# Kernel tuning notes

Hardware: AMD Instinct MI355X
Metric: run time of the kernel (lower is better)

Reference implementation:

```python
import jax, jax.numpy as jnp
import numpy as np

NC = 2            # num_classes
CONF_THR = 0.7
IOU_THR = 0.2

_PI, _PJ = np.triu_indices(9, k=1)   # 36 candidate edge directions for min-area rect


def _decode_level(out, stride):
    # out: [C,h,w]; scale (x,y) channels by stride and add the pixel grid, flatten to [h*w, C]
    C, h, w = out.shape
    gw = (stride * jnp.arange(w, dtype=out.dtype))[None, :]
    gh = (stride * jnp.arange(h, dtype=out.dtype))[:, None]
    out = out.at[NC + 1].set(out[NC + 1] * stride + gw)
    out = out.at[NC + 2].set(out[NC + 2] * stride + gh)
    return out.reshape(C, -1).T


def _min_area_polygons(pts18):
    # pts18: (N,18) interleaved (a,b) coordinate pairs of 9 points.
    # Min-area enclosing rectangle: optimal rect is aligned with some point-pair direction;
    # brute-force all 36 pairs (superset of hull edges) -> exact result, fully vectorized.
    P = pts18.reshape(-1, 9, 2)                       # (N,9,2)
    d = P[:, _PJ] - P[:, _PI]                         # (N,36,2)
    nrm = jnp.sqrt(jnp.sum(d * d, -1) + 1e-12)
    c, s = d[..., 0] / nrm, d[..., 1] / nrm           # (N,36)
    a, b = P[..., 0][:, None, :], P[..., 1][:, None, :]   # (N,1,9)
    u = a * c[..., None] + b * s[..., None]           # rotate by -theta
    v = -a * s[..., None] + b * c[..., None]
    umin, umax = u.min(-1), u.max(-1)
    vmin, vmax = v.min(-1), v.max(-1)
    area = (umax - umin) * (vmax - vmin)              # (N,36)
    k = jnp.argmin(area, 1)[:, None]
    tk = lambda z: jnp.take_along_axis(z, k, 1)[:, 0]
    c, s, umin, umax, vmin, vmax = map(tk, (c, s, umin, umax, vmin, vmax))
    cu = jnp.stack([umin, umax, umax, umin], -1)      # rect corners in rotated frame
    cv = jnp.stack([vmin, vmin, vmax, vmax], -1)
    ca = cu * c[:, None] - cv * s[:, None]            # rotate back
    cb = cu * s[:, None] + cv * c[:, None]
    return jnp.stack([ca, cb], -1).reshape(-1, 8)     # (N,8) interleaved corners


def _points_in_quad(pts, quad):
    # pts (M,2), quad (4,2) convex with consistent winding -> (M,) bool
    e = jnp.roll(quad, -1, 0) - quad
    r = pts[:, None, :] - quad[None]
    cr = e[None, :, 0] * r[..., 1] - e[None, :, 1] * r[..., 0]
    return (cr >= 0).all(-1) | (cr <= 0).all(-1)


def _box_decoder(rect):
    # rect (N,8) -> (N,5) [cx, cy, w, h, angle]; y_first=True convention from the source
    w = jnp.sqrt((rect[:, 0] - rect[:, 2]) ** 2 + (rect[:, 1] - rect[:, 3]) ** 2)
    h = jnp.sqrt((rect[:, 4] - rect[:, 2]) ** 2 + (rect[:, 5] - rect[:, 3]) ** 2)
    cx = rect[:, 1:8:2].sum(1) * 0.25
    cy = rect[:, 0:8:2].sum(1) * 0.25
    ang = jnp.arctan((rect[:, 0] - rect[:, 2]) / (rect[:, 1] - rect[:, 3]))
    return jnp.stack([cx, cy, w, h, ang], -1)


def _rbox_corners(b):
    cx, cy, w, h, a = b[0], b[1], b[2], b[3], b[4]
    cs, sn = jnp.cos(a), jnp.sin(a)
    lx = jnp.array([-0.5, 0.5, 0.5, -0.5]) * w
    ly = jnp.array([-0.5, -0.5, 0.5, 0.5]) * h
    return jnp.stack([cx + lx * cs - ly * sn, cy + lx * sn + ly * cs], -1)  # (4,2)


def _quad_inter_area(A, B):
    # exact intersection area of two convex quads A,B (4,2):
    # candidates = corners of each inside the other + all 16 edge-edge intersections,
    # sorted by angle around their centroid, masked shoelace.
    inA = _points_in_quad(B, A)
    inB = _points_in_quad(A, B)
    rA = jnp.roll(A, -1, 0) - A
    rB = jnp.roll(B, -1, 0) - B
    qp = B[None] - A[:, None]                                  # (4,4,2)
    den = rA[:, None, 0] * rB[None, :, 1] - rA[:, None, 1] * rB[None, :, 0]
    dsafe = jnp.where(jnp.abs(den) < 1e-9, 1e-9, den)
    t = (qp[..., 0] * rB[None, :, 1] - qp[..., 1] * rB[None, :, 0]) / dsafe
    uu = (qp[..., 0] * rA[:, None, 1] - qp[..., 1] * rA[:, None, 0]) / dsafe
    okx = (jnp.abs(den) > 1e-9) & (t >= 0) & (t <= 1) & (uu >= 0) & (uu <= 1)
    X = A[:, None] + t[..., None] * rA[:, None]
    pts = jnp.concatenate([A, B, X.reshape(16, 2)], 0)          # (24,2)
    val = jnp.concatenate([inB, inA, okx.reshape(16)], 0)
    n = val.sum()
    cen = jnp.sum(jnp.where(val[:, None], pts, 0.0), 0) / jnp.maximum(n, 1)
    rel = pts - cen
    ang = jnp.where(val, jnp.arctan2(rel[:, 1], rel[:, 0]), 1e9)
    o = jnp.argsort(ang)
    rp, vs = rel[o], val[o]
    rp = jnp.where(vs[:, None], rp, rp[0])   # invalid slots -> first valid vertex (zero-area edges)
    nx = jnp.roll(rp, -1, 0)
    area = 0.5 * jnp.abs(jnp.sum(rp[:, 0] * nx[:, 1] - rp[:, 1] * nx[:, 0]))
    return jnp.where(n >= 3, area, 0.0)


def _forward(out3, out4, out5, off1_l3, off1_l4, off1_l5, offf_l3, offf_l4, offf_l5):
    outs = jnp.concatenate([_decode_level(out3[0], 4),
                            _decode_level(out4[0], 8),
                            _decode_level(out5[0], 16)], 0)          # (N, NC+3)
    flat = lambda z: z[0].reshape(18, -1).T
    off1 = jnp.concatenate([flat(off1_l3), flat(off1_l4), flat(off1_l5)], 0)
    offf = jnp.concatenate([flat(offf_l3), flat(offf_l4), flat(offf_l5)], 0) + off1
    N = outs.shape[0]
    x, y = outs[:, NC + 1], outs[:, NC + 2]
    offf = offf + jnp.tile(jnp.stack([y, x], -1), (1, 9))            # (y,x) interleaved, 9 points
    xs, ys = offf[:, 1:18:2], offf[:, 0:18:2]
    area = (xs.max(1) - xs.min(1)) * (ys.max(1) - ys.min(1)) / 40.0
    conf = outs[:, 0]
    conf_mask = conf > CONF_THR * jax.nn.sigmoid(area)
    rect = _min_area_polygons(offf)                                  # (N,8)
    boxes5 = _box_decoder(rect)                                      # (N,5)
    corners = jax.vmap(_rbox_corners)(boxes5)                        # (N,4,2)
    areas5 = boxes5[:, 2] * boxes5[:, 3]
    position = outs[:, NC + 1:]                                      # (N,2) = (x,y)
    pts_yx = jnp.stack([position[:, 1], position[:, 0]], -1)         # (y,x), matches rect plane
    quads = rect.reshape(N, 4, 2)
    order = jnp.argsort(jnp.where(conf_mask, conf, -jnp.inf))[::-1]

    def step(carry, i):
        suppressed, keep = carry
        active = jnp.logical_not(suppressed[i])
        keep = keep.at[i].set(active)
        inside = _points_in_quad(pts_yx, quads[i])                   # points_in_polygons
        inter = jax.vmap(lambda C: _quad_inter_area(corners[i], C))(corners)
        iou = inter / (areas5[i] + areas5 - inter + 1e-9)            # box_iou_rotated
        suppressed = suppressed | (active & (inside | (iou >= IOU_THR)))
        return (suppressed, keep), None

    init = (jnp.logical_not(conf_mask), jnp.zeros(N, dtype=bool))
    (_, keep), _ = jax.lax.scan(step, init, order)

    cls = outs[:, 1:NC + 1]
    maxc = cls.max(1)
    masks = jnp.stack([keep & (cls[:, i] == maxc) for i in range(NC)], 0)  # (NC,N)
    cnt = masks.sum(1)
    result = jnp.where(masks[:, :, None], position[None], 0.0)             # (NC,N,2) padded
    rect_out = rect * keep[:, None].astype(rect.dtype)                     # (N,8) padded
    return cnt, result, rect_out


def setup_inputs() -> dict:
    key = jax.random.key(0)
    shapes = [("out3", (1, NC + 3, 32, 32)), ("out4", (1, NC + 3, 16, 16)), ("out5", (1, NC + 3, 8, 8)),
              ("off1_l3", (1, 18, 32, 32)), ("off1_l4", (1, 18, 16, 16)), ("off1_l5", (1, 18, 8, 8)),
              ("offf_l3", (1, 18, 32, 32)), ("offf_l4", (1, 18, 16, 16)), ("offf_l5", (1, 18, 8, 8))]
    ks = jax.random.split(key, len(shapes))
    return {n: jax.random.normal(k, s, dtype=jnp.float32) for (n, s), k in zip(shapes, ks)}


def reference(out3, out4, out5, off1_l3, off1_l4, off1_l5, offf_l3, offf_l4, offf_l5):
    return _forward(out3, out4, out5, off1_l3, off1_l4, off1_l5, offf_l3, offf_l4, offf_l5)
```

## Files before the change

kernel.cpp:

```cpp
#include <hip/hip_runtime.h>
#include <math.h>

#define N_DET 1344
#define MW_MAX 8
#define T2S 9
#define QCAP 2048


__device__ __forceinline__ bool pt_in_quad4(const float* qx, const float* qy,
                                            float px, float py) {
    bool allp = true, alln = true;
#pragma unroll
    for (int k = 0; k < 4; k++) {
        int k1 = (k + 1) & 3;
        float ex = qx[k1] - qx[k], ey = qy[k1] - qy[k];
        float rx = px - qx[k],     ry = py - qy[k];
        float cr = ex * ry - ey * rx;
        allp = allp && (cr >= 0.f);
        alln = alln && (cr <= 0.f);
    }
    return allp || alln;
}

__device__ float quad_inter_area(const float* Ax, const float* Ay,
                                 const float* Bx, const float* By) {
    float px[24], py[24];
    unsigned vmask = 0;
    int n = 0;
#pragma unroll
    for (int k = 0; k < 4; k++) {
        px[k] = Ax[k]; py[k] = Ay[k];
        if (pt_in_quad4(Bx, By, Ax[k], Ay[k])) { vmask |= 1u << k; n++; }
    }
#pragma unroll
    for (int k = 0; k < 4; k++) {
        px[4 + k] = Bx[k]; py[4 + k] = By[k];
        if (pt_in_quad4(Ax, Ay, Bx[k], By[k])) { vmask |= 1u << (4 + k); n++; }
    }
#pragma unroll
    for (int k = 0; k < 4; k++) {
        int k1 = (k + 1) & 3;
        float rax = Ax[k1] - Ax[k], ray = Ay[k1] - Ay[k];
#pragma unroll
        for (int l = 0; l < 4; l++) {
            int l1 = (l + 1) & 3;
            float rbx = Bx[l1] - Bx[l], rby = By[l1] - By[l];
            float qpx = Bx[l] - Ax[k],  qpy = By[l] - Ay[k];
            float den = rax * rby - ray * rbx;
            float ad  = fabsf(den);
            float dsafe = (ad < 1e-9f) ? 1e-9f : den;
            float t = (qpx * rby - qpy * rbx) / dsafe;
            float u = (qpx * ray - qpy * rax) / dsafe;
            bool ok = (ad > 1e-9f) && t >= 0.f && t <= 1.f && u >= 0.f && u <= 1.f;
            int id = 8 + k * 4 + l;
            px[id] = Ax[k] + t * rax;
            py[id] = Ay[k] + t * ray;
            if (ok) { vmask |= 1u << id; n++; }
        }
    }
    float cx = 0.f, cy = 0.f;
#pragma unroll
    for (int m = 0; m < 24; m++)
        if ((vmask >> m) & 1u) { cx += px[m]; cy += py[m]; }
    int mx = (n < 1) ? 1 : n;
    cx = cx / (float)mx;
    cy = cy / (float)mx;

    unsigned long long key[32];
    float sx[32], sy[32];
#pragma unroll
    for (int m = 0; m < 24; m++) {
        float rx = px[m] - cx, ry = py[m] - cy;
        float a = ((vmask >> m) & 1u) ? atan2f(ry, rx) : 1e9f;
        unsigned u = __float_as_uint(a);
        u = (u & 0x80000000u) ? ~u : (u | 0x80000000u);
        key[m] = (((unsigned long long)u) << 6) | (unsigned)m;
        sx[m] = rx; sy[m] = ry;
    }
#pragma unroll
    for (int m = 24; m < 32; m++) { key[m] = ~0ull; sx[m] = 0.f; sy[m] = 0.f; }

#pragma unroll
    for (int k = 2; k <= 32; k <<= 1) {
#pragma unroll
        for (int j = k >> 1; j > 0; j >>= 1) {
#pragma unroll
            for (int t = 0; t < 32; t++) {
                int l = t ^ j;
                if (l > t) {
                    bool up = ((t & k) == 0);
                    bool sw = up ? (key[t] > key[l]) : (key[t] < key[l]);
                    if (sw) {
                        unsigned long long tk = key[t]; key[t] = key[l]; key[l] = tk;
                        float tx = sx[t]; sx[t] = sx[l]; sx[l] = tx;
                        float ty = sy[t]; sy[t] = sy[l]; sy[l] = ty;
                    }
                }
            }
        }
    }

    unsigned ut = __float_as_uint(1e9f) | 0x80000000u;
    unsigned long long kt = ((unsigned long long)ut) << 6;
    float fx = sx[0], fy = sy[0];
    float qx2[24], qy2[24];
#pragma unroll
    for (int m = 0; m < 24; m++) {
        bool v = key[m] < kt;
        qx2[m] = v ? sx[m] : fx;
        qy2[m] = v ? sy[m] : fy;
    }
    float ssum = 0.f;
#pragma unroll
    for (int m = 0; m < 24; m++) {
        int m1 = (m + 1) % 24;
        ssum += qx2[m] * qy2[m1] - qy2[m] * qx2[m1];
    }
    float area = 0.5f * fabsf(ssum);
    return (n >= 3) ? area : 0.f;
}

__device__ bool iou_suppress_c(const float* __restrict__ co_cor,
                               const float* __restrict__ co_a5, int p, int q) {
    float Axr[4], Ayr[4], Bxr[4], Byr[4];
#pragma unroll
    for (int k = 0; k < 4; k++) {
        Axr[k] = co_cor[p * 8 + 2 * k]; Ayr[k] = co_cor[p * 8 + 2 * k + 1];
        Bxr[k] = co_cor[q * 8 + 2 * k]; Byr[k] = co_cor[q * 8 + 2 * k + 1];
    }
    float inter = quad_inter_area(Axr, Ayr, Bxr, Byr);
    float iou = inter / (co_a5[p] + co_a5[q] - inter + 1e-9f);
    return iou >= 0.2f;
}

__device__ __forceinline__ int sum_mcount(const int* __restrict__ mcount_w) {
    int M = 0;
#pragma unroll
    for (int k = 0; k < 21; k++) M += mcount_w[k];
    return M;
}

__global__ void k_decode(const float* __restrict__ out3, const float* __restrict__ out4,
                         const float* __restrict__ out5,
                         const float* __restrict__ o1l3, const float* __restrict__ o1l4,
                         const float* __restrict__ o1l5,
                         const float* __restrict__ ofl3, const float* __restrict__ ofl4,
                         const float* __restrict__ ofl5,
                         float* keyArr, float* cls0, float* cls1, float* xx, float* yy,
                         float* a5, float* ccx, float* ccy, float* rr,
                         float* rect, float* cor, int* mcount_w) {
    int n = blockIdx.x * blockDim.x + threadIdx.x;
    if (n >= N_DET) return;
    const float *out, *o1, *of;
    int w, idx; float stride;
    if (n < 1024)      { out = out3; o1 = o1l3; of = ofl3; w = 32; idx = n;        stride = 4.f; }
    else if (n < 1280) { out = out4; o1 = o1l4; of = ofl4; w = 16; idx = n - 1024; stride = 8.f; }
    else               { out = out5; o1 = o1l5; of = ofl5; w = 8;  idx = n - 1280; stride = 16.f; }
    int hw = w * w;
    int row = idx / w, col = idx % w;
    float cf = out[0 * hw + idx];
    float c0 = out[1 * hw + idx];
    float c1 = out[2 * hw + idx];
    float x  = out[3 * hw + idx] * stride + stride * (float)col;
    float y  = out[4 * hw + idx] * stride + stride * (float)row;

    float Pa[9], Pb[9];
    float minb = INFINITY, maxb = -INFINITY, mina = INFINITY, maxa = -INFINITY;
#pragma unroll
    for (int k = 0; k < 9; k++) {
        float a = of[(2 * k) * hw + idx]     + o1[(2 * k) * hw + idx]     + y;
        float b = of[(2 * k + 1) * hw + idx] + o1[(2 * k + 1) * hw + idx] + x;
        Pa[k] = a; Pb[k] = b;
        mina = fminf(mina, a); maxa = fmaxf(maxa, a);
        minb = fminf(minb, b); maxb = fmaxf(maxb, b);
    }
    float area = (maxb - minb) * (maxa - mina) / 40.0f;
    float sg = 1.0f / (1.0f + expf(-area));
    int m = (cf > 0.7f * sg) ? 1 : 0;

    float best = INFINITY, bc = 0.f, bs = 0.f;
    float bumin = 0.f, bumax = 0.f, bvmin = 0.f, bvmax = 0.f;
#pragma unroll
    for (int i = 0; i < 9; i++) {
#pragma unroll
        for (int j = i + 1; j < 9; j++) {
            float d0 = Pa[j] - Pa[i], d1 = Pb[j] - Pb[i];
            float nr = sqrtf(d0 * d0 + d1 * d1 + 1e-12f);
            float c = d0 / nr, s = d1 / nr;
            float umin = INFINITY, umax = -INFINITY, vmin = INFINITY, vmax = -INFINITY;
#pragma unroll
            for (int k = 0; k < 9; k++) {
                float u =  Pa[k] * c + Pb[k] * s;
                float v = -Pa[k] * s + Pb[k] * c;
                umin = fminf(umin, u); umax = fmaxf(umax, u);
                vmin = fminf(vmin, v); vmax = fmaxf(vmax, v);
            }
            float ar = (umax - umin) * (vmax - vmin);
            if (ar < best) { best = ar; bc = c; bs = s;
                             bumin = umin; bumax = umax; bvmin = vmin; bvmax = vmax; }
        }
    }
    float cu[4] = {bumin, bumax, bumax, bumin};
    float cv[4] = {bvmin, bvmin, bvmax, bvmax};
    float r8[8];
#pragma unroll
    for (int k = 0; k < 4; k++) {
        r8[2 * k]     = cu[k] * bc - cv[k] * bs;
        r8[2 * k + 1] = cu[k] * bs + cv[k] * bc;
    }
    float w5 = sqrtf((r8[0] - r8[2]) * (r8[0] - r8[2]) + (r8[1] - r8[3]) * (r8[1] - r8[3]));
    float h5 = sqrtf((r8[4] - r8[2]) * (r8[4] - r8[2]) + (r8[5] - r8[3]) * (r8[5] - r8[3]));
    float cx = (r8[1] + r8[3] + r8[5] + r8[7]) * 0.25f;
    float cy = (r8[0] + r8[2] + r8[4] + r8[6]) * 0.25f;
    float ang = atanf((r8[0] - r8[2]) / (r8[1] - r8[3]));
    float cs = cosf(ang), sn = sinf(ang);
    const float lxs[4] = {-0.5f, 0.5f, 0.5f, -0.5f};
    const float lys[4] = {-0.5f, -0.5f, 0.5f, 0.5f};
#pragma unroll
    for (int k = 0; k < 4; k++) {
        cor[n * 8 + 2 * k]     = cx + lxs[k] * w5 * cs - lys[k] * h5 * sn;
        cor[n * 8 + 2 * k + 1] = cy + lxs[k] * w5 * sn + lys[k] * h5 * cs;
    }
#pragma unroll
    for (int k = 0; k < 8; k++) rect[n * 8 + k] = r8[k];
    keyArr[n] = m ? cf : -INFINITY;
    cls0[n] = c0; cls1[n] = c1;
    xx[n] = x; yy[n] = y; a5[n] = w5 * h5;
    ccx[n] = cx; ccy[n] = cy;
    rr[n] = 0.5f * sqrtf(w5 * w5 + h5 * h5);
    unsigned long long mb = __ballot(m != 0);
    if ((threadIdx.x & 63) == 0) mcount_w[n >> 6] = (int)__popcll(mb);
}

__global__ __launch_bounds__(256) void k_order(
        const float* __restrict__ keyArr,
        const float* __restrict__ xx, const float* __restrict__ yy,
        const float* __restrict__ a5, const float* __restrict__ ccx,
        const float* __restrict__ ccy, const float* __restrict__ rr,
        const float* __restrict__ rect, const float* __restrict__ cor,
        int* order,
        float* co_ccx, float* co_ccy, float* co_rr, float* co_a5,
        float* co_xx, float* co_yy, float* co_rect, float* co_cor) {
    int lane = threadIdx.x & 63;
    int b = blockIdx.x * 4 + (threadIdx.x >> 6);
    float ki = keyArr[b];
    int rank = 0;
    for (int j = lane; j < N_DET; j += 64) {
        float kj = keyArr[j];
        rank += ((kj > ki) || (kj == ki && j > b)) ? 1 : 0;
    }
    for (int off = 32; off; off >>= 1) rank += __shfl_down(rank, off, 64);
    rank = __shfl(rank, 0, 64);
    if (lane == 0)           order[rank] = b;
    if (lane < 8)            co_cor[rank * 8 + lane]        = cor[b * 8 + lane];
    else if (lane < 16)      co_rect[rank * 8 + (lane - 8)] = rect[b * 8 + (lane - 8)];
    else if (lane == 16)     co_ccx[rank] = ccx[b];
    else if (lane == 17)     co_ccy[rank] = ccy[b];
    else if (lane == 18)     co_rr[rank]  = rr[b];
    else if (lane == 19)     co_a5[rank]  = a5[b];
    else if (lane == 20)     co_xx[rank]  = xx[b];
    else if (lane == 21)     co_yy[rank]  = yy[b];
}

__global__ __launch_bounds__(256) void k_pairs(
        const float* __restrict__ co_rect, const float* __restrict__ co_cor,
        const float* __restrict__ co_a5,
        const float* __restrict__ co_xx, const float* __restrict__ co_yy,
        const float* __restrict__ co_ccx, const float* __restrict__ co_ccy,
        const float* __restrict__ co_rr,
        const int* __restrict__ mcount_w, unsigned long long* __restrict__ S2) {
    __shared__ unsigned int queue[QCAP];
    __shared__ int qn;
    int M = sum_mcount(mcount_w);
    int MW = (M + 63) >> 6;
    bool fast = (MW <= MW_MAX);
    int tid = threadIdx.x;
    int lane = tid & 63;
    if (tid == 0) qn = 0;
    __syncthreads();

    if (M > 0) {
        int gwave = (blockIdx.x * 256 + tid) >> 6;
        int nwave = (gridDim.x * 256) >> 6;
        int total = M * MW;
        for (int t = gwave; t < total; t += nwave) {
            int p = t / MW;
            int w = t - p * MW;
            int q = w * 64 + lane;
            bool valid = q < M;
            int qc = valid ? q : 0;

            float cbi = co_ccx[p], cai = co_ccy[p], ri = co_rr[p];
            float pjy = co_yy[qc], pjx = co_xx[qc];
            float da = pjy - cai, db = pjx - cbi;
            float rin = ri + 0.1f;
            bool inside = false;
            if (da * da + db * db <= rin * rin) {
                float qxr[4], qyr[4];
#pragma unroll
                for (int k = 0; k < 4; k++) { qxr[k] = co_rect[p * 8 + 2 * k]; qyr[k] = co_rect[p * 8 + 2 * k + 1]; }
                inside = pt_in_quad4(qxr, qyr, pjy, pjx);
            }
            bool bit = valid && inside;
            unsigned long long bb = __ballot(bit);

            float ex = cbi - co_ccx[qc], ey = cai - co_ccy[qc];
            float rs = ri + co_rr[qc] + 0.1f;
            bool needy = valid && (q != p) && !bit && (ex * ex + ey * ey <= rs * rs);

            if (fast) {
                if (lane == 0) S2[p * MW + w] = bb;
                unsigned long long pm = __ballot(needy);
                if (pm) {
                    int cw = __popcll(pm);
                    int base = 0;
                    if (lane == 0) base = atomicAdd(&qn, cw);
                    base = __shfl(base, 0, 64);
                    if (needy) {
                        int pos = base + __popcll(pm & ((1ull << lane) - 1ull));
                        if (pos < QCAP) {
                            queue[pos] = ((unsigned)p << 11) | (unsigned)q;
                        } else {
                            __threadfence();
                            if (iou_suppress_c(co_cor, co_a5, p, q))
                                atomicOr(&S2[p * MW + w], 1ull << (q & 63));
                        }
                    }
                }
            } else {
                bool supp = needy && iou_suppress_c(co_cor, co_a5, p, q);
                unsigned long long sb = __ballot(supp);
                if (lane == 0) S2[p * MW + w] = bb | sb;
            }
        }
    }
    __syncthreads();

    if (M > 0 && fast) {
        int cnt = qn; if (cnt > QCAP) cnt = QCAP;
        for (int t = tid; t < cnt; t += 256) {
            unsigned v = queue[t];
            int p = (int)(v >> 11), q = (int)(v & 2047u);
            if (iou_suppress_c(co_cor, co_a5, p, q))
                atomicOr(&S2[p * MW + (q >> 6)], 1ull << (q & 63));
        }
    }
}

__global__ __launch_bounds__(512) void k_scan_out(
    const float* __restrict__ cls0, const float* __restrict__ cls1,
    const float* __restrict__ xx, const float* __restrict__ yy,
    const float* __restrict__ rect,
    const int* __restrict__ order, const int* __restrict__ mcount_w,
    const unsigned long long* __restrict__ S2, float* __restrict__ out) {
    __shared__ unsigned long long T2[512 * T2S];
    __shared__ unsigned long long Kfin[MW_MAX];
    __shared__ unsigned int keep32[(N_DET + 31) / 32];
    __shared__ int cnt_s[2];
    int tid = threadIdx.x;
    int lane = tid & 63, wid = tid >> 6;
    int M = sum_mcount(mcount_w);
    int MW = (M + 63) >> 6;
    for (int t = tid; t < (N_DET + 31) / 32; t += 512) keep32[t] = 0u;
    if (tid < 2) cnt_s[tid] = 0;
    if (tid < MW_MAX) Kfin[tid] = 0ull;
    __syncthreads();

    if (M > 0 && MW <= MW_MAX) {
        for (int blk = wid; blk < MW * MW; blk += 8) {
            int wp = blk / MW, wq = blk - wp * MW;
            int pp = wp * 64 + lane;
            unsigned long long x = (pp < M) ? S2[pp * MW + wq] : 0ull;
#pragma unroll
            for (int b = 0; b < 64; b++) {
                unsigned long long bb = __ballot((x >> b) & 1ull);
                if (lane == b) T2[(wq * 64 + b) * T2S + wp] = bb;
            }
        }
        __syncthreads();

        if (wid == 0) {
            unsigned long long kw[MW_MAX];
            unsigned long long pmask = lane ? ((1ull << lane) - 1ull) : 0ull;
#pragma unroll
            for (int k = 0; k < MW_MAX; k++) {
                if (k < MW) {
                    int q = k * 64 + lane;
                    const unsigned long long* row = &T2[q * T2S];
                    unsigned long long base = 0ull;
#pragma unroll
                    for (int w = 0; w < MW_MAX; w++)
                        if (w < k) base |= row[w] & kw[w];
                    unsigned long long rk = row[k] & pmask;
                    bool qv = q < M;
                    int lo = k * 64;
                    unsigned long long cur =
                        (M - lo >= 64) ? ~0ull : ((1ull << (M - lo)) - 1ull);
                    for (int guard = 0; guard < 66; guard++) {
                        bool nb = qv && ((base | (rk & cur)) == 0ull);
                        unsigned long long nw = __ballot(nb);
                        if (nw == cur) break;
                        cur = nw;
                    }
                    kw[k] = cur;
                }
            }
            if (lane == 0) {
#pragma unroll
                for (int w = 0; w < MW_MAX; w++) Kfin[w] = (w < MW) ? kw[w] : 0ull;
            }
        }
        __syncthreads();
        for (int t = tid; t < M; t += 512) {
            if ((Kfin[t >> 6] >> (t & 63)) & 1ull) {
                int i = order[t];
                atomicOr(&keep32[i >> 5], 1u << (i & 31));
            }
        }
    } else if (M > 0) {
        if (wid == 0) {
            unsigned long long rem = 0ull;
            int lo = lane * 64;
            if (M > lo) rem = (M - lo >= 64) ? ~0ull : ((1ull << (M - lo)) - 1ull);
            for (int guard = 0; guard < N_DET; guard++) {
                unsigned long long vote = __ballot(rem != 0ull);
                if (!vote) break;
                int w = __builtin_ctzll(vote);
                unsigned long long wd = __shfl(rem, w, 64);
                int b = __builtin_ctzll(wd);
                int p = w * 64 + b;
                int i = order[p];
                if (lane == 0) atomicOr(&keep32[i >> 5], 1u << (i & 31));
                unsigned long long rowv = (lane < MW) ? S2[p * MW + lane] : 0ull;
                rem &= ~rowv;
                if (lane == w) rem &= ~(1ull << b);
            }
        }
    }
    __syncthreads();

    int c0 = 0, c1 = 0;
    for (int n = tid; n < N_DET; n += 512) {
        bool kp = (keep32[n >> 5] >> (n & 31)) & 1u;
        float a = cls0[n], b = cls1[n];
        float mxc = fmaxf(a, b);
        bool m0 = kp && (a == mxc);
        bool m1 = kp && (b == mxc);
        float x = xx[n], y = yy[n];
        out[2 + 0 * N_DET * 2 + n * 2 + 0] = m0 ? x : 0.f;
        out[2 + 0 * N_DET * 2 + n * 2 + 1] = m0 ? y : 0.f;
        out[2 + 1 * N_DET * 2 + n * 2 + 0] = m1 ? x : 0.f;
        out[2 + 1 * N_DET * 2 + n * 2 + 1] = m1 ? y : 0.f;
        float kf = kp ? 1.f : 0.f;
#pragma unroll
        for (int k = 0; k < 8; k++)
            out[2 + 2 * N_DET * 2 + n * 8 + k] = rect[n * 8 + k] * kf;
        c0 += m0 ? 1 : 0;
        c1 += m1 ? 1 : 0;
    }
    if (c0) atomicAdd(&cnt_s[0], c0);
    if (c1) atomicAdd(&cnt_s[1], c1);
    __syncthreads();
    if (tid == 0) { out[0] = (float)cnt_s[0]; out[1] = (float)cnt_s[1]; }
}

extern "C" void kernel_launch(void* const* d_in, const int* in_sizes, int n_in,
                              void* d_out, int out_size, void* d_ws, size_t ws_size,
                              hipStream_t stream) {
    const int N = N_DET;
    float* wsf = (float*)d_ws;

    const float* out3 = (const float*)d_in[0];
    const float* out4 = (const float*)d_in[1];
    const float* out5 = (const float*)d_in[2];
    const float* o1l3 = (const float*)d_in[3];
    const float* o1l4 = (const float*)d_in[4];
    const float* o1l5 = (const float*)d_in[5];
    const float* ofl3 = (const float*)d_in[6];
    const float* ofl4 = (const float*)d_in[7];
    const float* ofl5 = (const float*)d_in[8];
    float* out = (float*)d_out;

    float* keyArr = wsf + 0 * N;
    float* cls0   = wsf + 1 * N;
    float* cls1   = wsf + 2 * N;
    float* xx     = wsf + 3 * N;
    float* yy     = wsf + 4 * N;
    float* a5     = wsf + 5 * N;
    float* ccx    = wsf + 6 * N;
    float* ccy    = wsf + 7 * N;
    float* rr     = wsf + 8 * N;
    float* rect   = wsf + 9 * N;
    float* cor    = wsf + 17 * N;
    float* co_ccx = wsf + 25 * N;
    float* co_ccy = wsf + 26 * N;
    float* co_rr  = wsf + 27 * N;
    float* co_a5  = wsf + 28 * N;
    float* co_xx  = wsf + 29 * N;
    float* co_yy  = wsf + 30 * N;
    float* co_rect= wsf + 31 * N;
    float* co_cor = wsf + 39 * N;
    int* order    = (int*)(wsf + 47 * N);
    int* mcount_w = order + N;
    unsigned long long* S2 = (unsigned long long*)(wsf + 48 * N + 24);

    k_decode<<<(N + 255) / 256, 256, 0, stream>>>(out3, out4, out5, o1l3, o1l4, o1l5,
                                                  ofl3, ofl4, ofl5,
                                                  keyArr, cls0, cls1, xx, yy, a5,
                                                  ccx, ccy, rr, rect, cor, mcount_w);
    k_order<<<N / 4, 256, 0, stream>>>(keyArr, xx, yy, a5, ccx, ccy, rr, rect, cor,
                                       order,
                                       co_ccx, co_ccy, co_rr, co_a5, co_xx, co_yy,
                                       co_rect, co_cor);
    k_pairs<<<256, 256, 0, stream>>>(co_rect, co_cor, co_a5, co_xx, co_yy,
                                     co_ccx, co_ccy, co_rr, mcount_w, S2);
    k_scan_out<<<1, 512, 0, stream>>>(cls0, cls1, xx, yy, rect, order, mcount_w, S2, out);
}
```

Before: 123.4 us.

## Fuse pair-suppression and scan-output kernels with last-block completion counter

Merges the pair-suppression kernel and the single-block greedy scan/output kernel into one launch. Each block increments a global done counter after its pair work, and the last block to finish runs the scan and writes the output. The counter is reset in the decode kernel. This removes one kernel launch and its gap, at the cost of all pair blocks carrying a larger shared-memory allocation and the scan running with 256 threads instead of 512.

```diff
diff --git a/kernel.cpp b/kernel.cpp
--- a/kernel.cpp
+++ b/kernel.cpp
@@ -5,6 +5,7 @@
 #define MW_MAX 8
 #define T2S 9
 #define QCAP 2048
+#define PAIR_BLOCKS 256
 
 
 __device__ __forceinline__ bool pt_in_quad4(const float* qx, const float* qy,
@@ -148,9 +149,10 @@
                          const float* __restrict__ ofl5,
                          float* keyArr, float* cls0, float* cls1, float* xx, float* yy,
                          float* a5, float* ccx, float* ccy, float* rr,
-                         float* rect, float* cor, int* mcount_w) {
+                         float* rect, float* cor, int* mcount_w, int* done) {
     int n = blockIdx.x * blockDim.x + threadIdx.x;
     if (n >= N_DET) return;
+    if (n == 0) *done = 0;
     const float *out, *o1, *of;
     int w, idx; float stride;
     if (n < 1024)      { out = out3; o1 = o1l3; of = ofl3; w = 32; idx = n;        stride = 4.f; }
@@ -262,20 +264,32 @@
     else if (lane == 21)     co_yy[rank]  = yy[b];
 }
 
-__global__ __launch_bounds__(256) void k_pairs(
+__global__ __launch_bounds__(256) void k_pairs_scan(
         const float* __restrict__ co_rect, const float* __restrict__ co_cor,
         const float* __restrict__ co_a5,
         const float* __restrict__ co_xx, const float* __restrict__ co_yy,
         const float* __restrict__ co_ccx, const float* __restrict__ co_ccy,
         const float* __restrict__ co_rr,
-        const int* __restrict__ mcount_w, unsigned long long* __restrict__ S2) {
+        const float* __restrict__ cls0, const float* __restrict__ cls1,
+        const float* __restrict__ xx, const float* __restrict__ yy,
+        const float* __restrict__ rect,
+        const int* __restrict__ order, const int* __restrict__ mcount_w,
+        unsigned long long* __restrict__ S2, int* __restrict__ done,
+        float* __restrict__ out) {
     __shared__ unsigned int queue[QCAP];
     __shared__ int qn;
+    __shared__ int is_last;
+    __shared__ unsigned long long T2[512 * T2S];
+    __shared__ unsigned long long Kfin[MW_MAX];
+    __shared__ unsigned int keep32[(N_DET + 31) / 32];
+    __shared__ int cnt_s[2];
+
     int M = sum_mcount(mcount_w);
     int MW = (M + 63) >> 6;
     bool fast = (MW <= MW_MAX);
     int tid = threadIdx.x;
     int lane = tid & 63;
+    int wid = tid >> 6;
     if (tid == 0) qn = 0;
     __syncthreads();
 
@@ -345,29 +359,24 @@
                 atomicOr(&S2[p * MW + (q >> 6)], 1ull << (q & 63));
         }
     }
-}
-
-__global__ __launch_bounds__(512) void k_scan_out(
-    const float* __restrict__ cls0, const float* __restrict__ cls1,
-    const float* __restrict__ xx, const float* __restrict__ yy,
-    const float* __restrict__ rect,
-    const int* __restrict__ order, const int* __restrict__ mcount_w,
-    const unsigned long long* __restrict__ S2, float* __restrict__ out) {
-    __shared__ unsigned long long T2[512 * T2S];
-    __shared__ unsigned long long Kfin[MW_MAX];
-    __shared__ unsigned int keep32[(N_DET + 31) / 32];
-    __shared__ int cnt_s[2];
-    int tid = threadIdx.x;
-    int lane = tid & 63, wid = tid >> 6;
-    int M = sum_mcount(mcount_w);
-    int MW = (M + 63) >> 6;
-    for (int t = tid; t < (N_DET + 31) / 32; t += 512) keep32[t] = 0u;
+
+    __syncthreads();
+    __threadfence();
+    if (tid == 0) {
+        int old = atomicAdd(done, 1);
+        is_last = (old == (int)gridDim.x - 1) ? 1 : 0;
+    }
+    __syncthreads();
+    if (!is_last) return;
+    __threadfence();
+
+    for (int t = tid; t < (N_DET + 31) / 32; t += 256) keep32[t] = 0u;
     if (tid < 2) cnt_s[tid] = 0;
     if (tid < MW_MAX) Kfin[tid] = 0ull;
     __syncthreads();
 
-    if (M > 0 && MW <= MW_MAX) {
-        for (int blk = wid; blk < MW * MW; blk += 8) {
+    if (M > 0 && fast) {
+        for (int blk = wid; blk < MW * MW; blk += 4) {
             int wp = blk / MW, wq = blk - wp * MW;
             int pp = wp * 64 + lane;
             unsigned long long x = (pp < M) ? S2[pp * MW + wq] : 0ull;
@@ -411,7 +420,7 @@
             }
         }
         __syncthreads();
-        for (int t = tid; t < M; t += 512) {
+        for (int t = tid; t < M; t += 256) {
             if ((Kfin[t >> 6] >> (t & 63)) & 1ull) {
                 int i = order[t];
                 atomicOr(&keep32[i >> 5], 1u << (i & 31));
@@ -440,7 +449,7 @@
     __syncthreads();
 
     int c0 = 0, c1 = 0;
-    for (int n = tid; n < N_DET; n += 512) {
+    for (int n = tid; n < N_DET; n += 256) {
         bool kp = (keep32[n >> 5] >> (n & 31)) & 1u;
         float a = cls0[n], b = cls1[n];
         float mxc = fmaxf(a, b);
@@ -502,17 +511,19 @@
     float* co_cor = wsf + 39 * N;
     int* order    = (int*)(wsf + 47 * N);
     int* mcount_w = order + N;
+    int* done     = mcount_w + 21;
     unsigned long long* S2 = (unsigned long long*)(wsf + 48 * N + 24);
 
     k_decode<<<(N + 255) / 256, 256, 0, stream>>>(out3, out4, out5, o1l3, o1l4, o1l5,
                                                   ofl3, ofl4, ofl5,
                                                   keyArr, cls0, cls1, xx, yy, a5,
-                                                  ccx, ccy, rr, rect, cor, mcount_w);
+                                                  ccx, ccy, rr, rect, cor, mcount_w, done);
     k_order<<<N / 4, 256, 0, stream>>>(keyArr, xx, yy, a5, ccx, ccy, rr, rect, cor,
                                        order,
                                        co_ccx, co_ccy, co_rr, co_a5, co_xx, co_yy,
                                        co_rect, co_cor);
-    k_pairs<<<256, 256, 0, stream>>>(co_rect, co_cor, co_a5, co_xx, co_yy,
-                                     co_ccx, co_ccy, co_rr, mcount_w, S2);
-    k_scan_out<<<1, 512, 0, stream>>>(cls0, cls1, xx, yy, rect, order, mcount_w, S2, out);
-}
+    k_pairs_scan<<<PAIR_BLOCKS, 256, 0, stream>>>(co_rect, co_cor, co_a5, co_xx, co_yy,
+                                                  co_ccx, co_ccy, co_rr,
+                                                  cls0, cls1, xx, yy, rect,
+                                                  order, mcount_w, S2, done, out);
+}
```

After: 160.2 us. +29.8%, slower.
